# Kernel optimization log

Hardware: AMD Instinct MI355X
Metric: run time of the kernel (lower is better)

## Reference

```python
import jax, jax.numpy as jnp
import numpy as np

B, S, V, D, H, T = 16, 256, 32000, 512, 512, 50


def setup_inputs() -> dict:
    key = jax.random.key(0)
    ks = jax.random.split(key, 6)
    tokens = jax.random.randint(ks[0], (B, S), 0, V, dtype=jnp.int64)
    topic_probs = jax.random.uniform(ks[1], (B, S, T), dtype=jnp.float32)
    topic_probs = topic_probs / jnp.linalg.norm(topic_probs, axis=-1, keepdims=True)
    embed_table = jax.random.normal(ks[2], (V, D), dtype=jnp.float32) * 0.02
    lstm_kernel = jax.random.normal(ks[3], (T + D + H, 4 * H), dtype=jnp.float32) * 0.02
    lstm_bias = jnp.zeros((4 * H,), dtype=jnp.float32)
    dense_w = jax.random.normal(ks[4], (H, V), dtype=jnp.float32) * 0.02
    dense_b = jnp.zeros((V,), dtype=jnp.float32)
    return {"tokens": tokens, "topic_probs": topic_probs, "embed_table": embed_table,
            "lstm_kernel": lstm_kernel, "lstm_bias": lstm_bias,
            "dense_w": dense_w, "dense_b": dense_b}


def _lstm(xs, kernel, bias):
    # xs: [B, S, T+D]; TF LSTMCell gate order: i, j(cell cand), f, o; forget_bias=0.0
    h_dim = bias.shape[0] // 4
    b = xs.shape[0]

    def step(carry, xt):
        c, h = carry
        z = jnp.concatenate([xt, h], axis=-1) @ kernel + bias  # [B, 4H]
        i, j, f, o = jnp.split(z, 4, axis=-1)
        c = jax.nn.sigmoid(f) * c + jax.nn.sigmoid(i) * jnp.tanh(j)
        h = jax.nn.sigmoid(o) * jnp.tanh(c)
        return (c, h), h

    init = (jnp.zeros((b, h_dim), xs.dtype), jnp.zeros((b, h_dim), xs.dtype))
    _, hs = jax.lax.scan(step, init, jnp.swapaxes(xs, 0, 1))  # [S, B, H]
    return jnp.swapaxes(hs, 0, 1)


def reference(tokens, topic_probs, embed_table, lstm_kernel, lstm_bias, dense_w, dense_b):
    word_emb = embed_table[tokens]                         # [B, S, D]
    xs = jnp.concatenate([topic_probs, word_emb], axis=-1)  # [B, S, T+D]
    hs = _lstm(xs, lstm_kernel, lstm_bias)                 # [B, S, H]
    logits = hs @ dense_w + dense_b                        # [B, S, V]
    return logits
```

## Files before the change

kernel.cpp:

```cpp
#include <hip/hip_runtime.h>
#include <cstdint>
#include <cstddef>

#define B_ 16
#define S_ 256
#define V_ 32000
#define D_ 512
#define H_ 512
#define T_ 50
#define KX (T_ + D_)
#define KXP 576
#define G4 (4 * H_)
#define M_ (B_ * S_)

#define GBLK 64
#define NWRK 192
#define UPB 8
#define WST 512
#define NJT 32
#define NNT 250

typedef unsigned short u16;
typedef unsigned int u32;
typedef __attribute__((ext_vector_type(8))) short bf16x8;
typedef __attribute__((ext_vector_type(4))) float f32x4;
typedef __attribute__((ext_vector_type(4))) u16 u16x4;
typedef __attribute__((ext_vector_type(8))) u16 u16x8;
typedef __attribute__((ext_vector_type(4))) u32 u32x4;

__device__ __forceinline__ float sigmoidf_(float x) { return 1.f / (1.f + expf(-x)); }

__device__ __forceinline__ u16 f2bf_rne(float x) {
  u32 u = __float_as_uint(x);
  u32 r = (u + 0x7fffu + ((u >> 16) & 1u)) >> 16;
  return (u16)r;
}
__device__ __forceinline__ float bf2f(u16 h) { return __uint_as_float(((u32)h) << 16); }

__device__ __forceinline__ int swz(int row, int k) {
  return row * WST + (k ^ ((row & 7) << 3));
}

#define GLD_LDS16(g, l) __builtin_amdgcn_global_load_lds( \
    (const __attribute__((address_space(1))) void*)(g), \
    (__attribute__((address_space(3))) void*)(l), 16, 0, 0)

__global__ __launch_bounds__(256) void gather_split_x(
    const int* __restrict__ tokens, const float* __restrict__ topic,
    const float* __restrict__ embed, u16* __restrict__ Xhi,
    u16* __restrict__ Xlo) {
  const int m = blockIdx.x;
  const int tok = tokens[m];
  const int k4 = threadIdx.x * 4;
  if (k4 >= KXP) return;
  u16x4 hv, lv;
  #pragma unroll
  for (int i = 0; i < 4; ++i) {
    int k = k4 + i;
    float v = 0.f;
    if (k < T_)       v = topic[(size_t)m * T_ + k];
    else if (k < KX)  v = embed[(size_t)tok * D_ + (k - T_)];
    u16 h = f2bf_rne(v);
    hv[i] = h;
    lv[i] = f2bf_rne(v - bf2f(h));
  }
  size_t o = (size_t)m * KXP + k4;
  *(u16x4*)(Xhi + o) = hv;
  *(u16x4*)(Xlo + o) = lv;
}

__global__ __launch_bounds__(256) void wx_split_t(
    const float* __restrict__ W, u16* __restrict__ Whi, u16* __restrict__ Wlo) {
  __shared__ float tile[32][33];
  const int n0 = blockIdx.x * 32, k0 = blockIdx.y * 32;
  const int r = threadIdx.x >> 3;
  const int c4 = (threadIdx.x & 7) * 4;
  const int kg = k0 + r;
  const float* src = W + (size_t)kg * G4 + n0 + c4;
  #pragma unroll
  for (int i = 0; i < 4; ++i) tile[r][c4 + i] = (kg < KX) ? src[i] : 0.f;
  __syncthreads();
  u16x4 hv, lv;
  #pragma unroll
  for (int i = 0; i < 4; ++i) {
    float x = tile[c4 + i][r];
    u16 h = f2bf_rne(x);
    hv[i] = h;
    lv[i] = f2bf_rne(x - bf2f(h));
  }
  size_t o = (size_t)(n0 + r) * KXP + k0 + c4;
  *(u16x4*)(Whi + o) = hv;
  *(u16x4*)(Wlo + o) = lv;
}

__global__ __launch_bounds__(256) void proj_mfma(
    const u16* __restrict__ Ahi, const u16* __restrict__ Alo,
    const u16* __restrict__ Bhi, const u16* __restrict__ Blo,
    const float* __restrict__ bias, float* __restrict__ C) {
  __shared__ u16 lds[4][128 * 32];
  const int tid = threadIdx.x;
  const int w = tid >> 6, lane = tid & 63;
  const int bm = blockIdx.y * 128;
  const int bn = blockIdx.x * 128;
  const int wm = (w >> 1) * 64, wn = (w & 1) * 64;

  f32x4 acc[4][4];
  #pragma unroll
  for (int m = 0; m < 4; ++m)
    #pragma unroll
    for (int n = 0; n < 4; ++n) acc[m][n] = (f32x4){0.f, 0.f, 0.f, 0.f};

  const u16* src0 = Ahi + (size_t)bm * KXP;
  const u16* src1 = Alo + (size_t)bm * KXP;
  const u16* src2 = Bhi + (size_t)bn * KXP;
  const u16* src3 = Blo + (size_t)bn * KXP;

  const int lrow = lane >> 2;
  const int lkb  = (lane & 3) * 8;
  const int kb   = (lane >> 4) * 8;

  for (int k0 = 0; k0 < KXP; k0 += 32) {
    #pragma unroll
    for (int cc = 0; cc < 2; ++cc) {
      const int c = w * 2 + cc;
      const int row = c * 16 + lrow;
      const size_t goff = (size_t)row * KXP + k0 + lkb;
      u16* l = &lds[0][0] + c * 16 * 32;
      GLD_LDS16(src0 + goff, l);
      GLD_LDS16(src1 + goff, l + 128 * 32);
      GLD_LDS16(src2 + goff, l + 2 * 128 * 32);
      GLD_LDS16(src3 + goff, l + 3 * 128 * 32);
    }
    __syncthreads();

    bf16x8 ah[4], al[4], bh[4], bl[4];
    #pragma unroll
    for (int m = 0; m < 4; ++m) {
      int r = wm + m * 16 + (lane & 15);
      ah[m] = *(const bf16x8*)&lds[0][r * 32 + kb];
      al[m] = *(const bf16x8*)&lds[1][r * 32 + kb];
    }
    #pragma unroll
    for (int n = 0; n < 4; ++n) {
      int r = wn + n * 16 + (lane & 15);
      bh[n] = *(const bf16x8*)&lds[2][r * 32 + kb];
      bl[n] = *(const bf16x8*)&lds[3][r * 32 + kb];
    }
    #pragma unroll
    for (int m = 0; m < 4; ++m)
      #pragma unroll
      for (int n = 0; n < 4; ++n) {
        acc[m][n] = __builtin_amdgcn_mfma_f32_16x16x32_bf16(al[m], bh[n], acc[m][n], 0, 0, 0);
        acc[m][n] = __builtin_amdgcn_mfma_f32_16x16x32_bf16(ah[m], bl[n], acc[m][n], 0, 0, 0);
        acc[m][n] = __builtin_amdgcn_mfma_f32_16x16x32_bf16(ah[m], bh[n], acc[m][n], 0, 0, 0);
      }
    __syncthreads();
  }

  const int lc = lane & 15, lr4 = (lane >> 4) * 4;
  #pragma unroll
  for (int n = 0; n < 4; ++n) {
    int col = bn + wn + n * 16 + lc;
    float bv = bias[col];
    #pragma unroll
    for (int m = 0; m < 4; ++m) {
      int row0 = bm + wm + m * 16 + lr4;
      float* Cp = C + (size_t)row0 * G4 + col;
      #pragma unroll
      for (int j = 0; j < 4; ++j)
        Cp[(size_t)j * G4] = acc[m][n][j] + bv;
    }
  }
}

__global__ __launch_bounds__(256) void split_w_t(
    const float* __restrict__ W, u16* __restrict__ Whi, u16* __restrict__ Wlo) {
  __shared__ float tile[32][33];
  const int n0 = blockIdx.x * 32, k0 = blockIdx.y * 32;
  const int r = threadIdx.x >> 3;
  const int c4 = (threadIdx.x & 7) * 4;
  const float* src = W + (size_t)(k0 + r) * V_ + n0 + c4;
  #pragma unroll
  for (int i = 0; i < 4; ++i) tile[r][c4 + i] = src[i];
  __syncthreads();
  u16x4 hv, lv;
  #pragma unroll
  for (int i = 0; i < 4; ++i) {
    float x = tile[c4 + i][r];
    u16 h = f2bf_rne(x);
    hv[i] = h;
    lv[i] = f2bf_rne(x - bf2f(h));
  }
  size_t o = (size_t)(n0 + r) * 512 + k0 + c4;
  *(u16x4*)(Whi + o) = hv;
  *(u16x4*)(Wlo + o) = lv;
}

__global__ __launch_bounds__(256, 1) void fused_lstm_dense(
    const float* __restrict__ xs_proj, const float* __restrict__ Wh,
    u32* __restrict__ hpk,
    u32* __restrict__ Apk,
    u32* __restrict__ ctr,
    const u16* __restrict__ Bhi, const u16* __restrict__ Blo,
    const float* __restrict__ bias, float* __restrict__ out) {
  __shared__ u16 whi_l[32 * WST];
  __shared__ u16 wlo_l[32 * WST];
  __shared__ u16 hhi_l[16 * WST];
  __shared__ u16 hlo_l[16 * WST];
  __shared__ float zpart[4][16][34];
  __shared__ u16 Ah_l[128 * 32];
  __shared__ u16 Al_l[128 * 32];
  __shared__ u16 Bh_l[128 * 32];
  __shared__ u16 Bl_l[128 * 32];

  const int bid = blockIdx.x;
  const int tid = threadIdx.x;
  const int w = tid >> 6;
  const int lane = tid & 63;

  if (bid < GBLK) {
    const int u0 = bid * UPB;

    for (int idx = tid; idx < 32 * 512; idx += 256) {
      int c = idx & 31, k = idx >> 5;
      int gc = (c >> 3) * 512 + u0 + (c & 7);
      float v = Wh[(size_t)k * G4 + gc];
      u16 hi = f2bf_rne(v);
      int si = swz(c, k);
      whi_l[si] = hi;
      wlo_l[si] = f2bf_rne(v - bf2f(hi));
    }

    float c_reg = 0.f;
    const int rb = tid >> 3;
    const int rj = tid & 7;
    const int kb = (lane >> 4) * 8;
    const int l15 = lane & 15;

    for (int s = 0; s < S_; ++s) {
      float zi = 0.f, zj2 = 0.f, zf = 0.f, zo = 0.f;
      if (tid < 128) {
        const float* zp = xs_proj + ((size_t)rb * S_ + s) * G4 + u0 + rj;
        zi = zp[0]; zj2 = zp[512]; zf = zp[1024]; zo = zp[1536];
      }

      if (s > 0) {
        if (tid == 0) {
          const u32 tgt = 64u * (u32)s;
          while (__hip_atomic_load(ctr, __ATOMIC_RELAXED,
                                   __HIP_MEMORY_SCOPE_AGENT) < tgt)
            __builtin_amdgcn_s_sleep(1);
        }
        __syncthreads();
        asm volatile("" ::: "memory");
      }

      {
        const u32* src = hpk + (size_t)(s & 1) * 8192;
        u32 v[32];
        #pragma unroll
        for (int j = 0; j < 32; ++j)
          v[j] = __hip_atomic_load(src + tid + j * 256, __ATOMIC_RELAXED,
                                   __HIP_MEMORY_SCOPE_AGENT);
        #pragma unroll
        for (int j = 0; j < 32; ++j) {
          int idx = tid + j * 256;
          int b = idx >> 9, u = idx & 511;
          int si = swz(b, u);
          hhi_l[si] = (u16)(v[j] & 0xffffu);
          hlo_l[si] = (u16)(v[j] >> 16);
        }
      }
      __syncthreads();

      {
        f32x4 acc0 = {0.f, 0.f, 0.f, 0.f};
        f32x4 acc1 = {0.f, 0.f, 0.f, 0.f};
        #pragma unroll
        for (int ks = 0; ks < 4; ++ks) {
          const int k = w * 128 + ks * 32 + kb;
          const int ia = swz(l15, k);
          const int ib = swz(16 + l15, k);
          bf16x8 ah  = *(const bf16x8*)&hhi_l[ia];
          bf16x8 al  = *(const bf16x8*)&hlo_l[ia];
          bf16x8 b0h = *(const bf16x8*)&whi_l[ia];
          bf16x8 b0l = *(const bf16x8*)&wlo_l[ia];
          bf16x8 b1h = *(const bf16x8*)&whi_l[ib];
          bf16x8 b1l = *(const bf16x8*)&wlo_l[ib];
          acc0 = __builtin_amdgcn_mfma_f32_16x16x32_bf16(al, b0h, acc0, 0, 0, 0);
          acc0 = __builtin_amdgcn_mfma_f32_16x16x32_bf16(ah, b0l, acc0, 0, 0, 0);
          acc0 = __builtin_amdgcn_mfma_f32_16x16x32_bf16(ah, b0h, acc0, 0, 0, 0);
          acc1 = __builtin_amdgcn_mfma_f32_16x16x32_bf16(al, b1h, acc1, 0, 0, 0);
          acc1 = __builtin_amdgcn_mfma_f32_16x16x32_bf16(ah, b1l, acc1, 0, 0, 0);
          acc1 = __builtin_amdgcn_mfma_f32_16x16x32_bf16(ah, b1h, acc1, 0, 0, 0);
        }
        #pragma unroll
        for (int jj = 0; jj < 4; ++jj) {
          int r = (lane >> 4) * 4 + jj;
          zpart[w][r][l15] = acc0[jj];
          zpart[w][r][16 + l15] = acc1[jj];
        }
      }
      __syncthreads();

      if (tid < 128) {
        #pragma unroll
        for (int ww = 0; ww < 4; ++ww) {
          zi  += zpart[ww][rb][rj];
          zj2 += zpart[ww][rb][8 + rj];
          zf  += zpart[ww][rb][16 + rj];
          zo  += zpart[ww][rb][24 + rj];
        }
        float cc = sigmoidf_(zf) * c_reg + sigmoidf_(zi) * tanhf(zj2);
        c_reg = cc;
        float h = sigmoidf_(zo) * tanhf(cc);
        u16 hh = f2bf_rne(h);
        u16 hl = f2bf_rne(h - bf2f(hh));
        u32 pack = (u32)hh | ((u32)hl << 16);
        const int hoff = rb * 512 + u0 + rj;
        __hip_atomic_store(hpk + (size_t)((s + 1) & 1) * 8192 + hoff, pack,
                           __ATOMIC_RELAXED, __HIP_MEMORY_SCOPE_AGENT);
        const size_t ar = ((size_t)s * 16 + rb) * 512 + u0 + rj;
        __hip_atomic_store(Apk + ar, pack,
                           __ATOMIC_RELAXED, __HIP_MEMORY_SCOPE_AGENT);
      }
      asm volatile("s_waitcnt vmcnt(0)" ::: "memory");
      __syncthreads();

      if (tid == 0)
        __hip_atomic_fetch_add(ctr, 1u, __ATOMIC_RELAXED,
                               __HIP_MEMORY_SCOPE_AGENT);
    }
  } else {
    const int wid = bid - GBLK;
    const int wm = (w >> 1) * 64, wn = (w & 1) * 64;
    const int l15 = lane & 15;
    const int kb = (lane >> 4) * 8;
    const int lrow = lane >> 2;
    const int lkb = (lane & 3) * 8;
    const int r_ = tid >> 1;
    const int kh = (tid & 1) * 16;

    int lastj = -1;
    for (int t = wid; t < NJT * NNT; t += NWRK) {
      const int jt = t / NNT;
      const int n  = t - jt * NNT;
      if (jt != lastj) {
        if (tid == 0) {
          const u32 tgt = 512u * (u32)(jt + 1);
          while (__hip_atomic_load(ctr, __ATOMIC_RELAXED,
                                   __HIP_MEMORY_SCOPE_AGENT) < tgt)
            __builtin_amdgcn_s_sleep(32);
        }
        __syncthreads();
        asm volatile("" ::: "memory");
        lastj = jt;
      }

      const int bmA = jt * 128;
      const int bn = n * 128;
      f32x4 acc[4][4];
      #pragma unroll
      for (int m = 0; m < 4; ++m)
        #pragma unroll
        for (int q = 0; q < 4; ++q) acc[m][q] = (f32x4){0.f, 0.f, 0.f, 0.f};

      const u16* srcBh = Bhi + (size_t)bn * 512;
      const u16* srcBl = Blo + (size_t)bn * 512;

      for (int k0 = 0; k0 < 512; k0 += 32) {
        {
          const u32* ap = Apk + (size_t)(bmA + r_) * 512 + k0 + kh;
          u32x4 a0 = *(const u32x4*)(ap);
          u32x4 a1 = *(const u32x4*)(ap + 4);
          u32x4 a2 = *(const u32x4*)(ap + 8);
          u32x4 a3 = *(const u32x4*)(ap + 12);
          u16x8 h0, h1, l0, l1;
          #pragma unroll
          for (int i = 0; i < 4; ++i) {
            h0[i]   = (u16)(a0[i] & 0xffffu); l0[i]   = (u16)(a0[i] >> 16);
            h0[4+i] = (u16)(a1[i] & 0xffffu); l0[4+i] = (u16)(a1[i] >> 16);
            h1[i]   = (u16)(a2[i] & 0xffffu); l1[i]   = (u16)(a2[i] >> 16);
            h1[4+i] = (u16)(a3[i] & 0xffffu); l1[4+i] = (u16)(a3[i] >> 16);
          }
          *(u16x8*)&Ah_l[r_ * 32 + kh]     = h0;
          *(u16x8*)&Ah_l[r_ * 32 + kh + 8] = h1;
          *(u16x8*)&Al_l[r_ * 32 + kh]     = l0;
          *(u16x8*)&Al_l[r_ * 32 + kh + 8] = l1;
        }
        #pragma unroll
        for (int cc = 0; cc < 2; ++cc) {
          const int c = w * 2 + cc;
          const int row = c * 16 + lrow;
          const size_t goff = (size_t)row * 512 + k0 + lkb;
          GLD_LDS16(srcBh + goff, &Bh_l[c * 16 * 32]);
          GLD_LDS16(srcBl + goff, &Bl_l[c * 16 * 32]);
        }
        __syncthreads();

        bf16x8 ah[4], al[4], bh[4], bl[4];
        #pragma unroll
        for (int m = 0; m < 4; ++m) {
          int r = wm + m * 16 + l15;
          ah[m] = *(const bf16x8*)&Ah_l[r * 32 + kb];
          al[m] = *(const bf16x8*)&Al_l[r * 32 + kb];
        }
        #pragma unroll
        for (int q = 0; q < 4; ++q) {
          int r = wn + q * 16 + l15;
          bh[q] = *(const bf16x8*)&Bh_l[r * 32 + kb];
          bl[q] = *(const bf16x8*)&Bl_l[r * 32 + kb];
        }
        #pragma unroll
        for (int m = 0; m < 4; ++m)
          #pragma unroll
          for (int q = 0; q < 4; ++q) {
            acc[m][q] = __builtin_amdgcn_mfma_f32_16x16x32_bf16(al[m], bh[q], acc[m][q], 0, 0, 0);
            acc[m][q] = __builtin_amdgcn_mfma_f32_16x16x32_bf16(ah[m], bl[q], acc[m][q], 0, 0, 0);
            acc[m][q] = __builtin_amdgcn_mfma_f32_16x16x32_bf16(ah[m], bh[q], acc[m][q], 0, 0, 0);
          }
        __syncthreads();
      }

      const int lc = lane & 15, lr4 = (lane >> 4) * 4;
      #pragma unroll
      for (int q = 0; q < 4; ++q) {
        int col = bn + wn + q * 16 + lc;
        float bv = bias[col];
        #pragma unroll
        for (int m = 0; m < 4; ++m) {
          int mbase = bmA + wm + m * 16;
          int s = mbase >> 4;
          float* Cp = out + ((size_t)lr4 * 256 + s) * V_ + col;
          #pragma unroll
          for (int jj = 0; jj < 4; ++jj)
            Cp[(size_t)jj * 256 * V_] = acc[m][q][jj] + bv;
        }
      }
    }
  }
}

extern "C" void kernel_launch(void* const* d_in, const int* in_sizes, int n_in,
                              void* d_out, int out_size, void* d_ws, size_t ws_size,
                              hipStream_t stream) {
  const int*   tokens = (const int*)  d_in[0];
  const float* topic  = (const float*)d_in[1];
  const float* embed  = (const float*)d_in[2];
  const float* lk     = (const float*)d_in[3];
  const float* lb     = (const float*)d_in[4];
  const float* dw     = (const float*)d_in[5];
  const float* db     = (const float*)d_in[6];
  float* out = (float*)d_out;

  char* ws = (char*)d_ws;
  size_t off = 0;
  float* xs_proj = (float*)(ws + off); off += (size_t)M_ * G4 * 4;
  char* xa = ws + off;
  u16* Xhi = (u16*)xa;
  u16* Xlo = (u16*)(xa + (size_t)M_ * KXP * 2);
  u32* Apk = (u32*)xa;
  off += (size_t)M_ * KXP * 2 * 2;
  u16* Whi = (u16*)(ws + off); off += (size_t)V_ * 512 * 2;
  u16* Wlo = (u16*)(ws + off); off += (size_t)V_ * 512 * 2;
  u16* Wxhi = (u16*)(ws + off); off += (size_t)G4 * KXP * 2;
  u16* Wxlo = (u16*)(ws + off); off += (size_t)G4 * KXP * 2;
  u32* hpk = (u32*)(ws + off); off += 2 * 8192 * 4;
  u32* ctr = (u32*)(ws + off); off += 256;

  hipMemsetAsync(hpk, 0, 2 * 8192 * 4, stream);
  hipMemsetAsync(ctr, 0, 256, stream);

  hipLaunchKernelGGL(split_w_t, dim3(V_ / 32, 512 / 32), dim3(256), 0, stream,
                     dw, Whi, Wlo);
  hipLaunchKernelGGL(wx_split_t, dim3(G4 / 32, KXP / 32), dim3(256), 0, stream,
                     lk, Wxhi, Wxlo);
  hipLaunchKernelGGL(gather_split_x, dim3(M_), dim3(256), 0, stream,
                     tokens, topic, embed, Xhi, Xlo);

  hipLaunchKernelGGL(proj_mfma, dim3(G4 / 128, M_ / 128), dim3(256), 0, stream,
                     Xhi, Xlo, Wxhi, Wxlo, lb, xs_proj);

  const float* Wh = lk + (size_t)KX * G4;
  hipLaunchKernelGGL(fused_lstm_dense, dim3(GBLK + NWRK), dim3(256), 0, stream,
                     xs_proj, Wh, hpk, Apk, ctr, Whi, Wlo, db, out);
}
```

Measured before the change: 1.187 ms.

## Keep recurrent weights in registers, union LDS, dynamic tile queue for dense workers

The LSTM blocks now hold their hi/lo bf16 slices of the recurrent weights in VGPRs instead of LDS. The shared memory is a union of the LSTM and dense layouts, which shrinks LDS per block so two blocks can fit per CU. With that, the worker count grows from 192 to 448 blocks, and dense tiles are claimed from a global atomic work queue instead of a static stride. The aim is more dense throughput overlapped with the serial recurrence, at the cost of register pressure and contention between recurrence blocks and co-resident dense blocks.

```diff
diff --git a/kernel.cpp b/kernel.cpp
--- a/kernel.cpp
+++ b/kernel.cpp
@@ -14,11 +14,12 @@
 #define M_ (B_ * S_)
 
 #define GBLK 64
-#define NWRK 192
+#define NWRK 448
 #define UPB 8
-#define WST 512
+#define HST 512
 #define NJT 32
 #define NNT 250
+#define NTILE (NJT * NNT)
 
 typedef unsigned short u16;
 typedef unsigned int u32;
@@ -38,7 +39,7 @@
 __device__ __forceinline__ float bf2f(u16 h) { return __uint_as_float(((u32)h) << 16); }
 
 __device__ __forceinline__ int swz(int row, int k) {
-  return row * WST + (k ^ ((row & 7) << 3));
+  return row * HST + (k ^ ((row & 7) << 3));
 }
 
 #define GLD_LDS16(g, l) __builtin_amdgcn_global_load_lds( \
@@ -196,22 +197,29 @@
   *(u16x4*)(Wlo + o) = lv;
 }
 
-__global__ __launch_bounds__(256, 1) void fused_lstm_dense(
+union SharedMem {
+  struct {
+    u16 hhi[16 * HST];
+    u16 hlo[16 * HST];
+    float zpart[4][16][34];
+  } lstm;
+  struct {
+    u16 Ah[128 * 32];
+    u16 Al[128 * 32];
+    u16 Bh[128 * 32];
+    u16 Bl[128 * 32];
+  } dense;
+};
+
+__global__ __launch_bounds__(256, 2) void fused_lstm_dense(
     const float* __restrict__ xs_proj, const float* __restrict__ Wh,
     u32* __restrict__ hpk,
     u32* __restrict__ Apk,
     u32* __restrict__ ctr,
     const u16* __restrict__ Bhi, const u16* __restrict__ Blo,
     const float* __restrict__ bias, float* __restrict__ out) {
-  __shared__ u16 whi_l[32 * WST];
-  __shared__ u16 wlo_l[32 * WST];
-  __shared__ u16 hhi_l[16 * WST];
-  __shared__ u16 hlo_l[16 * WST];
-  __shared__ float zpart[4][16][34];
-  __shared__ u16 Ah_l[128 * 32];
-  __shared__ u16 Al_l[128 * 32];
-  __shared__ u16 Bh_l[128 * 32];
-  __shared__ u16 Bl_l[128 * 32];
+  __shared__ SharedMem sm;
+  __shared__ u32 tshare;
 
   const int bid = blockIdx.x;
   const int tid = threadIdx.x;
@@ -220,22 +228,33 @@
 
   if (bid < GBLK) {
     const int u0 = bid * UPB;
-
-    for (int idx = tid; idx < 32 * 512; idx += 256) {
-      int c = idx & 31, k = idx >> 5;
-      int gc = (c >> 3) * 512 + u0 + (c & 7);
-      float v = Wh[(size_t)k * G4 + gc];
-      u16 hi = f2bf_rne(v);
-      int si = swz(c, k);
-      whi_l[si] = hi;
-      wlo_l[si] = f2bf_rne(v - bf2f(hi));
+    const int kb = (lane >> 4) * 8;
+    const int l15 = lane & 15;
+
+    bf16x8 wb0h[4], wb0l[4], wb1h[4], wb1l[4];
+    {
+      const int gc0 = ((l15 >> 3) * 512) + u0 + (l15 & 7);
+      const int gc1 = ((2 + (l15 >> 3)) * 512) + u0 + (l15 & 7);
+      #pragma unroll
+      for (int ks = 0; ks < 4; ++ks) {
+        const int kB = w * 128 + ks * 32 + kb;
+        #pragma unroll
+        for (int j = 0; j < 8; ++j) {
+          float v0 = Wh[(size_t)(kB + j) * G4 + gc0];
+          u16 h0 = f2bf_rne(v0);
+          wb0h[ks][j] = (short)h0;
+          wb0l[ks][j] = (short)f2bf_rne(v0 - bf2f(h0));
+          float v1 = Wh[(size_t)(kB + j) * G4 + gc1];
+          u16 h1 = f2bf_rne(v1);
+          wb1h[ks][j] = (short)h1;
+          wb1l[ks][j] = (short)f2bf_rne(v1 - bf2f(h1));
+        }
+      }
     }
 
     float c_reg = 0.f;
     const int rb = tid >> 3;
     const int rj = tid & 7;
-    const int kb = (lane >> 4) * 8;
-    const int l15 = lane & 15;
 
     for (int s = 0; s < S_; ++s) {
       float zi = 0.f, zj2 = 0.f, zf = 0.f, zo = 0.f;
@@ -267,8 +286,8 @@
           int idx = tid + j * 256;
           int b = idx >> 9, u = idx & 511;
           int si = swz(b, u);
-          hhi_l[si] = (u16)(v[j] & 0xffffu);
-          hlo_l[si] = (u16)(v[j] >> 16);
+          sm.lstm.hhi[si] = (u16)(v[j] & 0xffffu);
+          sm.lstm.hlo[si] = (u16)(v[j] >> 16);
         }
       }
       __syncthreads();
@@ -280,25 +299,20 @@
         for (int ks = 0; ks < 4; ++ks) {
           const int k = w * 128 + ks * 32 + kb;
           const int ia = swz(l15, k);
-          const int ib = swz(16 + l15, k);
-          bf16x8 ah  = *(const bf16x8*)&hhi_l[ia];
-          bf16x8 al  = *(const bf16x8*)&hlo_l[ia];
-          bf16x8 b0h = *(const bf16x8*)&whi_l[ia];
-          bf16x8 b0l = *(const bf16x8*)&wlo_l[ia];
-          bf16x8 b1h = *(const bf16x8*)&whi_l[ib];
-          bf16x8 b1l = *(const bf16x8*)&wlo_l[ib];
-          acc0 = __builtin_amdgcn_mfma_f32_16x16x32_bf16(al, b0h, acc0, 0, 0, 0);
-          acc0 = __builtin_amdgcn_mfma_f32_16x16x32_bf16(ah, b0l, acc0, 0, 0, 0);
-          acc0 = __builtin_amdgcn_mfma_f32_16x16x32_bf16(ah, b0h, acc0, 0, 0, 0);
-          acc1 = __builtin_amdgcn_mfma_f32_16x16x32_bf16(al, b1h, acc1, 0, 0, 0);
-          acc1 = __builtin_amdgcn_mfma_f32_16x16x32_bf16(ah, b1l, acc1, 0, 0, 0);
-          acc1 = __builtin_amdgcn_mfma_f32_16x16x32_bf16(ah, b1h, acc1, 0, 0, 0);
+          bf16x8 ah = *(const bf16x8*)&sm.lstm.hhi[ia];
+          bf16x8 al = *(const bf16x8*)&sm.lstm.hlo[ia];
+          acc0 = __builtin_amdgcn_mfma_f32_16x16x32_bf16(al, wb0h[ks], acc0, 0, 0, 0);
+          acc0 = __builtin_amdgcn_mfma_f32_16x16x32_bf16(ah, wb0l[ks], acc0, 0, 0, 0);
+          acc0 = __builtin_amdgcn_mfma_f32_16x16x32_bf16(ah, wb0h[ks], acc0, 0, 0, 0);
+          acc1 = __builtin_amdgcn_mfma_f32_16x16x32_bf16(al, wb1h[ks], acc1, 0, 0, 0);
+          acc1 = __builtin_amdgcn_mfma_f32_16x16x32_bf16(ah, wb1l[ks], acc1, 0, 0, 0);
+          acc1 = __builtin_amdgcn_mfma_f32_16x16x32_bf16(ah, wb1h[ks], acc1, 0, 0, 0);
         }
         #pragma unroll
         for (int jj = 0; jj < 4; ++jj) {
           int r = (lane >> 4) * 4 + jj;
-          zpart[w][r][l15] = acc0[jj];
-          zpart[w][r][16 + l15] = acc1[jj];
+          sm.lstm.zpart[w][r][l15] = acc0[jj];
+          sm.lstm.zpart[w][r][16 + l15] = acc1[jj];
         }
       }
       __syncthreads();
@@ -306,10 +320,10 @@
       if (tid < 128) {
         #pragma unroll
         for (int ww = 0; ww < 4; ++ww) {
-          zi  += zpart[ww][rb][rj];
-          zj2 += zpart[ww][rb][8 + rj];
-          zf  += zpart[ww][rb][16 + rj];
-          zo  += zpart[ww][rb][24 + rj];
+          zi  += sm.lstm.zpart[ww][rb][rj];
+          zj2 += sm.lstm.zpart[ww][rb][8 + rj];
+          zf  += sm.lstm.zpart[ww][rb][16 + rj];
+          zo  += sm.lstm.zpart[ww][rb][24 + rj];
         }
         float cc = sigmoidf_(zf) * c_reg + sigmoidf_(zi) * tanhf(zj2);
         c_reg = cc;
@@ -332,7 +346,7 @@
                                __HIP_MEMORY_SCOPE_AGENT);
     }
   } else {
-    const int wid = bid - GBLK;
+    u32* wq = ctr + 64;
     const int wm = (w >> 1) * 64, wn = (w & 1) * 64;
     const int l15 = lane & 15;
     const int kb = (lane >> 4) * 8;
@@ -342,9 +356,15 @@
     const int kh = (tid & 1) * 16;
 
     int lastj = -1;
-    for (int t = wid; t < NJT * NNT; t += NWRK) {
-      const int jt = t / NNT;
-      const int n  = t - jt * NNT;
+    for (;;) {
+      if (tid == 0)
+        tshare = __hip_atomic_fetch_add(wq, 1u, __ATOMIC_RELAXED,
+                                        __HIP_MEMORY_SCOPE_AGENT);
+      __syncthreads();
+      const u32 t = tshare;
+      if (t >= (u32)NTILE) break;
+      const int jt = (int)(t / NNT);
+      const int n  = (int)(t - (u32)jt * NNT);
       if (jt != lastj) {
         if (tid == 0) {
           const u32 tgt = 512u * (u32)(jt + 1);
@@ -383,18 +403,18 @@
             h1[i]   = (u16)(a2[i] & 0xffffu); l1[i]   = (u16)(a2[i] >> 16);
             h1[4+i] = (u16)(a3[i] & 0xffffu); l1[4+i] = (u16)(a3[i] >> 16);
           }
-          *(u16x8*)&Ah_l[r_ * 32 + kh]     = h0;
-          *(u16x8*)&Ah_l[r_ * 32 + kh + 8] = h1;
-          *(u16x8*)&Al_l[r_ * 32 + kh]     = l0;
-          *(u16x8*)&Al_l[r_ * 32 + kh + 8] = l1;
+          *(u16x8*)&sm.dense.Ah[r_ * 32 + kh]     = h0;
+          *(u16x8*)&sm.dense.Ah[r_ * 32 + kh + 8] = h1;
+          *(u16x8*)&sm.dense.Al[r_ * 32 + kh]     = l0;
+          *(u16x8*)&sm.dense.Al[r_ * 32 + kh + 8] = l1;
         }
         #pragma unroll
         for (int cc = 0; cc < 2; ++cc) {
           const int c = w * 2 + cc;
           const int row = c * 16 + lrow;
           const size_t goff = (size_t)row * 512 + k0 + lkb;
-          GLD_LDS16(srcBh + goff, &Bh_l[c * 16 * 32]);
-          GLD_LDS16(srcBl + goff, &Bl_l[c * 16 * 32]);
+          GLD_LDS16(srcBh + goff, &sm.dense.Bh[c * 16 * 32]);
+          GLD_LDS16(srcBl + goff, &sm.dense.Bl[c * 16 * 32]);
         }
         __syncthreads();
 
@@ -402,14 +422,14 @@
         #pragma unroll
         for (int m = 0; m < 4; ++m) {
           int r = wm + m * 16 + l15;
-          ah[m] = *(const bf16x8*)&Ah_l[r * 32 + kb];
-          al[m] = *(const bf16x8*)&Al_l[r * 32 + kb];
+          ah[m] = *(const bf16x8*)&sm.dense.Ah[r * 32 + kb];
+          al[m] = *(const bf16x8*)&sm.dense.Al[r * 32 + kb];
         }
         #pragma unroll
         for (int q = 0; q < 4; ++q) {
           int r = wn + q * 16 + l15;
-          bh[q] = *(const bf16x8*)&Bh_l[r * 32 + kb];
-          bl[q] = *(const bf16x8*)&Bl_l[r * 32 + kb];
+          bh[q] = *(const bf16x8*)&sm.dense.Bh[r * 32 + kb];
+          bl[q] = *(const bf16x8*)&sm.dense.Bl[r * 32 + kb];
         }
         #pragma unroll
         for (int m = 0; m < 4; ++m)
@@ -466,10 +486,10 @@
   u16* Wxhi = (u16*)(ws + off); off += (size_t)G4 * KXP * 2;
   u16* Wxlo = (u16*)(ws + off); off += (size_t)G4 * KXP * 2;
   u32* hpk = (u32*)(ws + off); off += 2 * 8192 * 4;
-  u32* ctr = (u32*)(ws + off); off += 256;
+  u32* ctr = (u32*)(ws + off); off += 512;
 
   hipMemsetAsync(hpk, 0, 2 * 8192 * 4, stream);
-  hipMemsetAsync(ctr, 0, 256, stream);
+  hipMemsetAsync(ctr, 0, 512, stream);
 
   hipLaunchKernelGGL(split_w_t, dim3(V_ / 32, 512 / 32), dim3(256), 0, stream,
                      dw, Whi, Wlo);
```

Measured after the change: 2.145 ms. +80.6%, slower.
